# Performance work log

Measured on AMD Instinct MI355X. Metric: run time of the kernel, lower is better.

Reference implementation:

```python
import jax, jax.numpy as jnp
import numpy as np

ALPHA = 0.2  # LeakyReLU negative slope
NEG_INF = -1e9


def setup_inputs() -> dict:
    key = jax.random.key(0)
    k1, k2, k3, k4 = jax.random.split(key, 4)
    B, N, IN, OUT = 8, 2048, 512, 32
    graph_input = jax.random.normal(k1, (B, N, IN), dtype=jnp.float32)
    adj = jax.random.randint(k2, (B, N, N), 0, 2, dtype=jnp.int32)
    W_fc = jax.random.normal(k3, (OUT, IN), dtype=jnp.float32) * (1.0 / np.sqrt(IN))
    W_attn = jax.random.normal(k4, (1, 2 * OUT), dtype=jnp.float32) * (1.0 / np.sqrt(2 * OUT))
    return {"graph_input": graph_input, "adj": adj, "W_fc": W_fc, "W_attn": W_attn}


def reference(graph_input, adj, W_fc, W_attn):
    # h: [B, N, 32]
    h = jnp.einsum('bni,oi->bno', graph_input, W_fc)
    out_dim = W_fc.shape[0]
    # attn_fc(cat(h_i, h_j)) is separable: a1.h_i + a2.h_j
    a1 = W_attn[0, :out_dim]   # [32]
    a2 = W_attn[0, out_dim:]   # [32]
    f1 = jnp.einsum('bno,o->bn', h, a1)  # [B, N]
    f2 = jnp.einsum('bno,o->bn', h, a2)  # [B, N]
    scores = jax.nn.leaky_relu(f1[:, :, None] + f2[:, None, :], negative_slope=ALPHA)  # [B,N,N]
    scores = jnp.where(adj == 0, NEG_INF, scores)
    attn = jax.nn.softmax(scores, axis=2)
    # NOTE: original multiplies attention with graph_input (not h)
    h_prime = jnp.einsum('bnm,bmi->bni', attn, graph_input)  # [B, N, IN]
    return jax.nn.elu(h_prime)  # concat=True path
```

## Files before the change

kernel.cpp:

```cpp
#include <hip/hip_runtime.h>
#include <hip/hip_bf16.h>

#define BATCH 8
#define NN    2048
#define FIN   512
#define FOUT  32
#define GALPHA 0.2f
#define NROW  128
#define NIT   32

typedef float  f32x4  __attribute__((ext_vector_type(4)));
typedef __bf16 bf16x8 __attribute__((ext_vector_type(8)));
typedef unsigned short u16;
typedef u16 u16x8 __attribute__((ext_vector_type(8)));

static __device__ __forceinline__ u16 f2bf(float f) {
    __hip_bfloat16 h = __float2bfloat16(f);
    union { __hip_bfloat16 h; u16 u; } c; c.h = h; return c.u;
}
static __device__ __forceinline__ float bf2f(u16 u) {
    union { u16 u; __hip_bfloat16 h; } c; c.u = u; return __bfloat162float(c.h);
}

__global__ __launch_bounds__(256) void k_prep(
    const float* __restrict__ x, const int* __restrict__ adj,
    const float* __restrict__ Wfc, const float* __restrict__ Wat,
    __hip_bfloat16* __restrict__ xt,
    float* __restrict__ f1, float* __restrict__ f2,
    unsigned int* __restrict__ bits)
{
    const int bx = blockIdx.x;
    const int tt = threadIdx.x;

    if (bx >= 256) {
        int row  = (bx - 256) * 4 + (tt >> 6);
        int lane = tt & 63;
        const int* p = adj + (size_t)row * NN + lane * 32;
        unsigned int bv = 0;
        #pragma unroll
        for (int j = 0; j < 8; j++) {
            int4 v = *(const int4*)(p + j * 4);
            bv |= (v.x != 0 ? 1u : 0u) << (j * 4 + 0);
            bv |= (v.y != 0 ? 1u : 0u) << (j * 4 + 1);
            bv |= (v.z != 0 ? 1u : 0u) << (j * 4 + 2);
            bv |= (v.w != 0 ? 1u : 0u) << (j * 4 + 3);
        }
        bits[(size_t)row * 64 + lane] = bv;
        return;
    }

    __shared__ u16 tile[64][72];
    __shared__ __align__(16) float w1s[FIN];
    __shared__ __align__(16) float w2s[FIN];

    const int b  = bx >> 5;
    const int mt = bx & 31;
    const int m0 = mt * 64;

    #pragma unroll
    for (int h = 0; h < 2; h++) {
        int i = tt + h * 256;
        float s1 = 0.f, s2 = 0.f;
        #pragma unroll
        for (int o = 0; o < FOUT; o++) {
            float wv = Wfc[o * FIN + i];
            s1 += wv * Wat[o];
            s2 += wv * Wat[FOUT + o];
        }
        w1s[i] = s1; w2s[i] = s2;
    }
    __syncthreads();

    const int mm  = tt >> 3;
    const int icl = (tt & 7) * 8;
    const float* xb = x + ((size_t)b * NN + m0) * FIN;
    float p1[2] = {0.f, 0.f}, p2[2] = {0.f, 0.f};

    for (int it = 0; it < 8; it++) {
        const int i0 = it * 64;
        f32x4 wA = *(const f32x4*)&w1s[i0 + icl];
        f32x4 wB = *(const f32x4*)&w1s[i0 + icl + 4];
        f32x4 wC = *(const f32x4*)&w2s[i0 + icl];
        f32x4 wD = *(const f32x4*)&w2s[i0 + icl + 4];
        #pragma unroll
        for (int h = 0; h < 2; h++) {
            int m = mm + h * 32;
            const f32x4* src = (const f32x4*)(xb + (size_t)m * FIN + i0 + icl);
            f32x4 v0 = src[0], v1 = src[1];
            u16x8 pk;
            float s1 = 0.f, s2 = 0.f;
            #pragma unroll
            for (int j = 0; j < 4; j++) {
                pk[j] = f2bf(v0[j]); pk[4 + j] = f2bf(v1[j]);
                s1 += v0[j] * wA[j] + v1[j] * wB[j];
                s2 += v0[j] * wC[j] + v1[j] * wD[j];
            }
            p1[h] += s1; p2[h] += s2;
            *(u16x8*)&tile[m][icl] = pk;
        }
        __syncthreads();
        __hip_bfloat16* xtb = xt + ((size_t)b * FIN + i0) * NN + m0;
        const int mc = (tt & 7) * 8;
        #pragma unroll
        for (int h = 0; h < 2; h++) {
            int ii = (tt >> 3) + h * 32;
            u16x8 v;
            #pragma unroll
            for (int j = 0; j < 8; j++) v[j] = tile[mc + j][ii];
            *(u16x8*)(xtb + (size_t)ii * NN + mc) = v;
        }
        if (it < 7) __syncthreads();
    }

    #pragma unroll
    for (int off = 1; off < 8; off <<= 1) {
        p1[0] += __shfl_xor(p1[0], off); p1[1] += __shfl_xor(p1[1], off);
        p2[0] += __shfl_xor(p2[0], off); p2[1] += __shfl_xor(p2[1], off);
    }
    if ((tt & 7) == 0) {
        size_t r0 = (size_t)b * NN + m0 + mm;
        f1[r0] = p1[0];      f1[r0 + 32] = p1[1];
        f2[r0] = p2[0];      f2[r0 + 32] = p2[1];
    }
}

__global__ __launch_bounds__(512, 2) void k_main(
    const unsigned int* __restrict__ bits, const __hip_bfloat16* __restrict__ xt,
    const float* __restrict__ f1, const float* __restrict__ f2,
    float* __restrict__ out)
{
    const int bx = blockIdx.x;
    const int b = bx & 7, rt = (bx >> 3) & 15, it = bx >> 7;
    const int n0 = rt * NROW;
    const int i0 = it * 256;
    const int tid = threadIdx.x;
    const int lane = tid & 63, wv = tid >> 6;
    const int quad = lane >> 4, l15 = lane & 15;

    __shared__ u16 At[2][NROW * 64];
    __shared__ float rs[NROW];

    const int grow = tid >> 2;
    const int q4   = tid & 3;
    const unsigned short* bp = (const unsigned short*)bits
                               + ((size_t)(b * NN) + n0 + grow) * 128 + q4;
    const float* f2p = f2 + b * NN + q4 * 16;
    const float  f1v = f1[b * NN + n0 + grow];
    const int swz = grow & 7;
    u16* wp0 = &At[0][grow * 64 + (((q4 * 2) ^ swz) * 8)];
    u16* wp1 = &At[0][grow * 64 + (((q4 * 2 + 1) ^ swz) * 8)];
    float rpart = 0.f;

    const __hip_bfloat16* xtp = xt + ((size_t)(b * FIN) + i0 + wv * 32 + l15) * NN + quad * 8;

    f32x4 acc[8][2];
    #pragma unroll
    for (int s = 0; s < 8; s++) { acc[s][0] = (f32x4){0,0,0,0}; acc[s][1] = (f32x4){0,0,0,0}; }

    auto gen = [&](int buf, unsigned int bv, const f32x4* fr) {
        u16x8 pk0, pk1;
        #pragma unroll
        for (int e = 0; e < 16; e++) {
            float s  = f1v + fr[e >> 2][e & 3];
            float ls = fmaxf(s, GALPHA * s);
            float ev = ((bv >> e) & 1u) ? __expf(ls) : 0.f;
            u16 hb = f2bf(ev);
            rpart += bf2f(hb);
            if (e < 8) pk0[e] = hb; else pk1[e - 8] = hb;
        }
        *(u16x8*)(wp0 + buf * (NROW * 64)) = pk0;
        *(u16x8*)(wp1 + buf * (NROW * 64)) = pk1;
    };

    {
        unsigned int b0 = bp[0];
        f32x4 g0[4];
        #pragma unroll
        for (int j = 0; j < 4; j++) g0[j] = *(const f32x4*)(f2p + j * 4);
        gen(0, b0, g0);
    }
    unsigned int brng[2];
    f32x4 frng[2][4];
    brng[1] = bp[4];
    #pragma unroll
    for (int j = 0; j < 4; j++) frng[1][j] = *(const f32x4*)(f2p + 64 + j * 4);
    brng[0] = bp[8];
    #pragma unroll
    for (int j = 0; j < 4; j++) frng[0][j] = *(const f32x4*)(f2p + 128 + j * 4);

    bf16x8 Bc[2][2], Bn[2][2];
    #pragma unroll
    for (int ks = 0; ks < 2; ks++)
        #pragma unroll
        for (int c = 0; c < 2; c++)
            Bc[ks][c] = *(const bf16x8*)(xtp + ks * 32 + (size_t)(c * 16) * NN);
    __syncthreads();

    #pragma unroll 2
    for (int t = 0; t < NIT; t++) {
        const int cur = t & 1;
        if (t < NIT - 1) {
            const __hip_bfloat16* xk = xtp + (t + 1) * 64;
            #pragma unroll
            for (int ks = 0; ks < 2; ks++)
                #pragma unroll
                for (int c = 0; c < 2; c++)
                    Bn[ks][c] = *(const bf16x8*)(xk + ks * 32 + (size_t)(c * 16) * NN);
        }
        #pragma unroll
        for (int ks = 0; ks < 2; ks++) {
            #pragma unroll
            for (int s = 0; s < 8; s++) {
                const int row = s * 16 + l15;
                bf16x8 Af = *(const bf16x8*)&At[cur][row * 64 + (((ks * 4 + quad) ^ (row & 7)) * 8)];
                acc[s][0] = __builtin_amdgcn_mfma_f32_16x16x32_bf16(Af, Bc[ks][0], acc[s][0], 0, 0, 0);
                acc[s][1] = __builtin_amdgcn_mfma_f32_16x16x32_bf16(Af, Bc[ks][1], acc[s][1], 0, 0, 0);
            }
        }
        if (t < NIT - 1) {
            gen(1 - cur, brng[(t + 1) & 1], frng[(t + 1) & 1]);
            if (t < NIT - 2) {
                brng[t & 1] = bp[(t + 2) * 4];
                #pragma unroll
                for (int j = 0; j < 4; j++)
                    frng[t & 1][j] = *(const f32x4*)(f2p + (t + 2) * 64 + j * 4);
            }
        }
        asm volatile("s_waitcnt lgkmcnt(0)\ns_barrier" ::: "memory");
        #pragma unroll
        for (int ks = 0; ks < 2; ks++) {
            Bc[ks][0] = Bn[ks][0]; Bc[ks][1] = Bn[ks][1];
        }
    }

    rpart += __shfl_xor(rpart, 1);
    rpart += __shfl_xor(rpart, 2);
    if (q4 == 0) rs[grow] = 1.0f / rpart;
    __syncthreads();

    #pragma unroll
    for (int s = 0; s < 8; s++) {
        #pragma unroll
        for (int r = 0; r < 4; r++) {
            const int row = s * 16 + quad * 4 + r;
            const float inv = rs[row];
            float* op = out + ((size_t)b * NN + (n0 + row)) * FIN + i0 + wv * 32 + l15;
            #pragma unroll
            for (int c = 0; c < 2; c++) {
                float v = acc[s][c][r] * inv;
                v = v > 0.f ? v : (__expf(v) - 1.f);
                op[c * 16] = v;
            }
        }
    }
}

extern "C" void kernel_launch(void* const* d_in, const int* in_sizes, int n_in,
                              void* d_out, int out_size, void* d_ws, size_t ws_size,
                              hipStream_t stream) {
    const float* x   = (const float*)d_in[0];
    const int*   adj = (const int*)d_in[1];
    const float* Wfc = (const float*)d_in[2];
    const float* Wat = (const float*)d_in[3];
    float* out = (float*)d_out;

    float* f1 = (float*)d_ws;
    float* f2 = f1 + BATCH * NN;
    unsigned int* bits = (unsigned int*)(f2 + BATCH * NN);
    __hip_bfloat16* xt = (__hip_bfloat16*)(bits + (size_t)BATCH * NN * 64);

    hipLaunchKernelGGL(k_prep, dim3(4352), dim3(256), 0, stream,
                       x, adj, Wfc, Wat, xt, f1, f2, bits);
    hipLaunchKernelGGL(k_main, dim3(256),  dim3(512), 0, stream,
                       bits, xt, f1, f2, out);
}
```

Measured before the change: 294.7 us.

## Split prep kernel over feature chunks and fold adjacency packing into each block

The prep kernel grid moves from 256 transpose blocks (each looping over all 8 feature chunks) plus 4096 adjacency-packing blocks to 2048 uniform blocks. Each block handles one 64x64 tile of the bf16 transpose and also packs 8 adjacency rows into bitmasks. f1 and f2 partial dot products are now accumulated with atomicAdd across feature chunks, which needs a memset beforehand. This is meant to raise parallelism and balance in the memory-bound prep stage, at the cost of atomics and an extra memset launch.

```diff
diff --git a/kernel.cpp b/kernel.cpp
--- a/kernel.cpp
+++ b/kernel.cpp
@@ -30,36 +30,16 @@
     unsigned int* __restrict__ bits)
 {
     const int bx = blockIdx.x;
+    const int it = bx & 7, mt = (bx >> 3) & 31, b = bx >> 8;
+    const int m0 = mt * 64, i0 = it * 64;
     const int tt = threadIdx.x;
 
-    if (bx >= 256) {
-        int row  = (bx - 256) * 4 + (tt >> 6);
-        int lane = tt & 63;
-        const int* p = adj + (size_t)row * NN + lane * 32;
-        unsigned int bv = 0;
-        #pragma unroll
-        for (int j = 0; j < 8; j++) {
-            int4 v = *(const int4*)(p + j * 4);
-            bv |= (v.x != 0 ? 1u : 0u) << (j * 4 + 0);
-            bv |= (v.y != 0 ? 1u : 0u) << (j * 4 + 1);
-            bv |= (v.z != 0 ? 1u : 0u) << (j * 4 + 2);
-            bv |= (v.w != 0 ? 1u : 0u) << (j * 4 + 3);
-        }
-        bits[(size_t)row * 64 + lane] = bv;
-        return;
-    }
-
     __shared__ u16 tile[64][72];
-    __shared__ __align__(16) float w1s[FIN];
-    __shared__ __align__(16) float w2s[FIN];
-
-    const int b  = bx >> 5;
-    const int mt = bx & 31;
-    const int m0 = mt * 64;
-
-    #pragma unroll
-    for (int h = 0; h < 2; h++) {
-        int i = tt + h * 256;
+    __shared__ __align__(16) float w1s[64];
+    __shared__ __align__(16) float w2s[64];
+
+    if (tt < 64) {
+        const int i = i0 + tt;
         float s1 = 0.f, s2 = 0.f;
         #pragma unroll
         for (int o = 0; o < FOUT; o++) {
@@ -67,51 +47,34 @@
             s1 += wv * Wat[o];
             s2 += wv * Wat[FOUT + o];
         }
-        w1s[i] = s1; w2s[i] = s2;
+        w1s[tt] = s1; w2s[tt] = s2;
     }
     __syncthreads();
 
     const int mm  = tt >> 3;
     const int icl = (tt & 7) * 8;
-    const float* xb = x + ((size_t)b * NN + m0) * FIN;
-    float p1[2] = {0.f, 0.f}, p2[2] = {0.f, 0.f};
-
-    for (int it = 0; it < 8; it++) {
-        const int i0 = it * 64;
-        f32x4 wA = *(const f32x4*)&w1s[i0 + icl];
-        f32x4 wB = *(const f32x4*)&w1s[i0 + icl + 4];
-        f32x4 wC = *(const f32x4*)&w2s[i0 + icl];
-        f32x4 wD = *(const f32x4*)&w2s[i0 + icl + 4];
-        #pragma unroll
-        for (int h = 0; h < 2; h++) {
-            int m = mm + h * 32;
-            const f32x4* src = (const f32x4*)(xb + (size_t)m * FIN + i0 + icl);
-            f32x4 v0 = src[0], v1 = src[1];
-            u16x8 pk;
-            float s1 = 0.f, s2 = 0.f;
-            #pragma unroll
-            for (int j = 0; j < 4; j++) {
-                pk[j] = f2bf(v0[j]); pk[4 + j] = f2bf(v1[j]);
-                s1 += v0[j] * wA[j] + v1[j] * wB[j];
-                s2 += v0[j] * wC[j] + v1[j] * wD[j];
-            }
-            p1[h] += s1; p2[h] += s2;
-            *(u16x8*)&tile[m][icl] = pk;
-        }
-        __syncthreads();
-        __hip_bfloat16* xtb = xt + ((size_t)b * FIN + i0) * NN + m0;
-        const int mc = (tt & 7) * 8;
-        #pragma unroll
-        for (int h = 0; h < 2; h++) {
-            int ii = (tt >> 3) + h * 32;
-            u16x8 v;
-            #pragma unroll
-            for (int j = 0; j < 8; j++) v[j] = tile[mc + j][ii];
-            *(u16x8*)(xtb + (size_t)ii * NN + mc) = v;
-        }
-        if (it < 7) __syncthreads();
-    }
-
+    const float* xb = x + ((size_t)b * NN + m0) * FIN + i0;
+    f32x4 wA = *(const f32x4*)&w1s[icl];
+    f32x4 wB = *(const f32x4*)&w1s[icl + 4];
+    f32x4 wC = *(const f32x4*)&w2s[icl];
+    f32x4 wD = *(const f32x4*)&w2s[icl + 4];
+    float p1[2], p2[2];
+    #pragma unroll
+    for (int h = 0; h < 2; h++) {
+        int m = mm + h * 32;
+        const f32x4* src = (const f32x4*)(xb + (size_t)m * FIN + icl);
+        f32x4 v0 = src[0], v1 = src[1];
+        u16x8 pk;
+        float s1 = 0.f, s2 = 0.f;
+        #pragma unroll
+        for (int j = 0; j < 4; j++) {
+            pk[j] = f2bf(v0[j]); pk[4 + j] = f2bf(v1[j]);
+            s1 += v0[j] * wA[j] + v1[j] * wB[j];
+            s2 += v0[j] * wC[j] + v1[j] * wD[j];
+        }
+        p1[h] = s1; p2[h] = s2;
+        *(u16x8*)&tile[m][icl] = pk;
+    }
     #pragma unroll
     for (int off = 1; off < 8; off <<= 1) {
         p1[0] += __shfl_xor(p1[0], off); p1[1] += __shfl_xor(p1[1], off);
@@ -119,8 +82,45 @@
     }
     if ((tt & 7) == 0) {
         size_t r0 = (size_t)b * NN + m0 + mm;
-        f1[r0] = p1[0];      f1[r0 + 32] = p1[1];
-        f2[r0] = p2[0];      f2[r0 + 32] = p2[1];
+        atomicAdd(&f1[r0], p1[0]);      atomicAdd(&f1[r0 + 32], p1[1]);
+        atomicAdd(&f2[r0], p2[0]);      atomicAdd(&f2[r0 + 32], p2[1]);
+    }
+    __syncthreads();
+    __hip_bfloat16* xtb = xt + ((size_t)b * FIN + i0) * NN + m0;
+    const int mc = (tt & 7) * 8;
+    #pragma unroll
+    for (int h = 0; h < 2; h++) {
+        int ii = (tt >> 3) + h * 32;
+        u16x8 v;
+        #pragma unroll
+        for (int j = 0; j < 8; j++) v[j] = tile[mc + j][ii];
+        *(u16x8*)(xtb + (size_t)ii * NN + mc) = v;
+    }
+
+    {
+        const int r = tt >> 5;
+        const int c = tt & 31;
+        const size_t row = (size_t)b * NN + m0 + it * 8 + r;
+        const int* p = adj + row * NN + c * 64;
+        unsigned int bv0 = 0, bv1 = 0;
+        #pragma unroll
+        for (int j = 0; j < 8; j++) {
+            int4 v = *(const int4*)(p + j * 4);
+            bv0 |= (v.x != 0 ? 1u : 0u) << (j * 4 + 0);
+            bv0 |= (v.y != 0 ? 1u : 0u) << (j * 4 + 1);
+            bv0 |= (v.z != 0 ? 1u : 0u) << (j * 4 + 2);
+            bv0 |= (v.w != 0 ? 1u : 0u) << (j * 4 + 3);
+        }
+        #pragma unroll
+        for (int j = 0; j < 8; j++) {
+            int4 v = *(const int4*)(p + 32 + j * 4);
+            bv1 |= (v.x != 0 ? 1u : 0u) << (j * 4 + 0);
+            bv1 |= (v.y != 0 ? 1u : 0u) << (j * 4 + 1);
+            bv1 |= (v.z != 0 ? 1u : 0u) << (j * 4 + 2);
+            bv1 |= (v.w != 0 ? 1u : 0u) << (j * 4 + 3);
+        }
+        uint2 wv; wv.x = bv0; wv.y = bv1;
+        *(uint2*)&bits[row * 64 + c * 2] = wv;
     }
 }
 
@@ -269,7 +269,8 @@
     unsigned int* bits = (unsigned int*)(f2 + BATCH * NN);
     __hip_bfloat16* xt = (__hip_bfloat16*)(bits + (size_t)BATCH * NN * 64);
 
-    hipLaunchKernelGGL(k_prep, dim3(4352), dim3(256), 0, stream,
+    hipMemsetAsync(f1, 0, (size_t)2 * BATCH * NN * sizeof(float), stream);
+    hipLaunchKernelGGL(k_prep, dim3(2048), dim3(256), 0, stream,
                        x, adj, Wfc, Wat, xt, f1, f2, bits);
     hipLaunchKernelGGL(k_main, dim3(256),  dim3(512), 0, stream,
                        bits, xt, f1, f2, out);
```

Result: faster. 285.8 us (-3.0%).
